# Kernel optimization log

Hardware: AMD Instinct MI355X
Metric: run time of the kernel (lower is better)

## Reference

```python
import jax, jax.numpy as jnp
import numpy as np

D, DK, DV, H, DFF = 1024, 64, 64, 16, 4096
B, LD, LE = 8, 1024, 1024
NEG = -1e9


def _ln(x, g, b, eps=1e-5):
    m = jnp.mean(x, axis=-1, keepdims=True)
    v = jnp.var(x, axis=-1, keepdims=True)
    return (x - m) / jnp.sqrt(v + eps) * g + b


def _mha(q_src, kv_src, wq, bq, wk, bk, wv, bv, mask):
    # wq/wk: [H, D, DK], wv: [H, D, DV]; per-head linear projections (with bias)
    Q = jnp.einsum('bld,hdk->bhlk', q_src, wq) + bq[:, None, :]
    K = jnp.einsum('bld,hdk->bhlk', kv_src, wk) + bk[:, None, :]
    V = jnp.einsum('bld,hdv->bhlv', kv_src, wv) + bv[:, None, :]
    s = jnp.einsum('bhqk,bhmk->bhqm', Q, K) / jnp.sqrt(jnp.asarray(DK, Q.dtype))
    if mask is not None:
        s = s + mask
    a = jax.nn.softmax(s, axis=-1)
    o = jnp.einsum('bhqm,bhmv->bhqv', a, V)  # [B,H,L,DV]
    b_, h_, l_, dv_ = o.shape
    return jnp.transpose(o, (0, 2, 1, 3)).reshape(b_, l_, h_ * dv_)


def setup_inputs() -> dict:
    key = jax.random.key(0)
    ks = jax.random.split(key, 24)
    sc = 0.02
    inp = {
        'decoder_embedding': jax.random.normal(ks[0], (B, LD, D), jnp.float32),
        'encoder_output': jax.random.normal(ks[1], (B, LE, D), jnp.float32),
        # masked (self) attention heads, stacked over H
        'm_wq': jax.random.normal(ks[2], (H, D, DK)) * sc,
        'm_bq': jnp.zeros((H, DK)),
        'm_wk': jax.random.normal(ks[3], (H, D, DK)) * sc,
        'm_bk': jnp.zeros((H, DK)),
        'm_wv': jax.random.normal(ks[4], (H, D, DV)) * sc,
        'm_bv': jnp.zeros((H, DV)),
        # cross attention heads
        'c_wq': jax.random.normal(ks[5], (H, D, DK)) * sc,
        'c_bq': jnp.zeros((H, DK)),
        'c_wk': jax.random.normal(ks[6], (H, D, DK)) * sc,
        'c_bk': jnp.zeros((H, DK)),
        'c_wv': jax.random.normal(ks[7], (H, D, DV)) * sc,
        'c_bv': jnp.zeros((H, DV)),
        # FFN
        'ff_w1': jax.random.normal(ks[8], (D, DFF)) * sc,
        'ff_b1': jnp.zeros((DFF,)),
        'ff_w2': jax.random.normal(ks[9], (DFF, D)) * sc,
        'ff_b2': jnp.zeros((D,)),
        # LayerNorms (ln2 reused for the third norm, as in the source)
        'ln1_g': jnp.ones((D,)), 'ln1_b': jnp.zeros((D,)),
        'ln2_g': jnp.ones((D,)), 'ln2_b': jnp.zeros((D,)),
    }
    return inp


def reference(decoder_embedding, encoder_output,
              m_wq, m_bq, m_wk, m_bk, m_wv, m_bv,
              c_wq, c_bq, c_wk, c_bk, c_wv, c_bv,
              ff_w1, ff_b1, ff_w2, ff_b2,
              ln1_g, ln1_b, ln2_g, ln2_b):
    Ld = decoder_embedding.shape[1]
    causal = jnp.where(jnp.tril(jnp.ones((Ld, Ld), bool)), 0.0, NEG)[None, None]
    # masked self-attention + residual + LN1
    sa = _mha(decoder_embedding, decoder_embedding, m_wq, m_bq, m_wk, m_bk, m_wv, m_bv, causal)
    x = _ln(decoder_embedding + sa, ln1_g, ln1_b)
    # cross-attention (Q from decoder, K/V from encoder) + residual + LN2
    ca = _mha(x, encoder_output, c_wq, c_bq, c_wk, c_bk, c_wv, c_bv, None)
    x = _ln(x + ca, ln2_g, ln2_b)
    # FFN + residual + LN2 again (source reuses layer_norm2)
    ff = jnp.maximum(x @ ff_w1 + ff_b1, 0.0) @ ff_w2 + ff_b2
    return _ln(x + ff, ln2_g, ln2_b)
```

## Files before the change

### kernel.cpp

```cpp
#include <hip/hip_runtime.h>
#include <hip/hip_bf16.h>
#include <cstdint>

typedef __bf16 bf16x8 __attribute__((ext_vector_type(8)));
typedef __bf16 bf16x4 __attribute__((ext_vector_type(4)));
typedef short  short4v __attribute__((ext_vector_type(4)));
typedef _Float16 f16x4 __attribute__((ext_vector_type(4)));
typedef float f32x4 __attribute__((ext_vector_type(4)));

union U128 { uint4 u; __bf16 h[8]; };
union U64  { uint2 u; __bf16 h[4]; };
union PV4  { uint2 u; bf16x4 b; short4v s; f16x4 f; };

#define DMODEL 1024
#define NHEAD  16
#define DHEAD  64

#if __has_builtin(__builtin_amdgcn_mfma_f32_16x16x16_bf16)
#define PV_F16 0
__device__ __forceinline__ f32x4 mfma16(PV4 a, PV4 b, f32x4 c) {
  return __builtin_amdgcn_mfma_f32_16x16x16_bf16(a.b, b.b, c, 0, 0, 0);
}
#elif __has_builtin(__builtin_amdgcn_mfma_f32_16x16x16bf16_1k)
#define PV_F16 0
__device__ __forceinline__ f32x4 mfma16(PV4 a, PV4 b, f32x4 c) {
  return __builtin_amdgcn_mfma_f32_16x16x16bf16_1k(a.s, b.s, c, 0, 0, 0);
}
#else
#define PV_F16 1
__device__ __forceinline__ f32x4 mfma16(PV4 a, PV4 b, f32x4 c) {
  return __builtin_amdgcn_mfma_f32_16x16x16f16(a.f, b.f, c, 0, 0, 0);
}
#endif

__device__ __forceinline__ uint16_t pv_bits(__bf16 v) {
#if PV_F16
  union { _Float16 f; uint16_t u; } x; x.f = (_Float16)(float)v; return x.u;
#else
  union { __bf16 b; uint16_t u; } x; x.b = v; return x.u;
#endif
}

__device__ __forceinline__ PV4 pack4(float a, float b, float c, float d) {
  PV4 r;
#if PV_F16
  r.f = (f16x4){(_Float16)a, (_Float16)b, (_Float16)c, (_Float16)d};
#else
  r.b = (bf16x4){(__bf16)a, (__bf16)b, (__bf16)c, (__bf16)d};
#endif
  return r;
}

__device__ __forceinline__ void async_copy16(const void* g, void* l) {
  __builtin_amdgcn_global_load_lds(
      (const __attribute__((address_space(1))) void*)g,
      (__attribute__((address_space(3))) void*)l, 16, 0, 0);
}

__global__ __launch_bounds__(256) void k_cast(const float* __restrict__ s,
    __bf16* __restrict__ d, int n) {
  int i = (blockIdx.x * 256 + threadIdx.x) * 4;
  if (i < n) {
    float4 v = *(const float4*)(s + i);
    U64 o;
    o.h[0] = (__bf16)v.x; o.h[1] = (__bf16)v.y;
    o.h[2] = (__bf16)v.z; o.h[3] = (__bf16)v.w;
    *(uint2*)(d + i) = o.u;
  }
}

__global__ __launch_bounds__(256) void k_pack(float* __restrict__ dst,
    const float* __restrict__ s0, const float* __restrict__ s1,
    const float* __restrict__ s2, int n) {
  int i = blockIdx.x * 256 + threadIdx.x;
  if (i < n) dst[i] = s0[i];
  else if (i < 2 * n) dst[i] = s1[i - n];
  else if (i < 3 * n) dst[i] = s2[i - 2 * n];
}

__global__ __launch_bounds__(256) void k_transpose(const float* __restrict__ src,
    __bf16* __restrict__ dst, int R, int C) {
  __shared__ __bf16 tile[32][33];
  src += (size_t)blockIdx.z * R * C;
  dst += (size_t)blockIdx.z * R * C;
  int c0 = blockIdx.x * 32, r0 = blockIdx.y * 32;
  int tx = threadIdx.x & 31, ty = threadIdx.x >> 5;
  for (int i = ty; i < 32; i += 8)
    tile[i][tx] = (__bf16)src[(size_t)(r0 + i) * C + (c0 + tx)];
  __syncthreads();
  for (int i = ty; i < 32; i += 8)
    dst[(size_t)(c0 + i) * R + (r0 + tx)] = tile[tx][i];
}

template<bool RELU, typename OutT>
__global__ __launch_bounds__(256, 3) void k_gemm(const __bf16* __restrict__ A,
    const __bf16* __restrict__ Bt, const float* __restrict__ bias,
    OutT* __restrict__ C, int M, int N, int K) {
  __shared__ __bf16 As[128][64];
  __shared__ __bf16 Bs[128][64];
  const int m0 = blockIdx.y * 128, n0 = blockIdx.x * 128;
  const int t = threadIdx.x;
  const int wave = t >> 6, lane = t & 63;
  const int wm = (wave & 1) * 64, wn = (wave >> 1) * 64;
  const int lrow = lane & 15, quad = lane >> 4;
  const int r8 = lane >> 3;
  const int gG = (lane & 7) ^ (r8 & 7);
  const __bf16* Ap[4]; const __bf16* Bp[4];
  __bf16* lA[4]; __bf16* lB[4];
  for (int j = 0; j < 4; j++) {
    int rr = wave * 8 + j * 32 + r8;
    Ap[j] = A  + (size_t)(m0 + rr) * K + gG * 8;
    Bp[j] = Bt + (size_t)(n0 + rr) * K + gG * 8;
    lA[j] = &As[wave * 8 + j * 32][0];
    lB[j] = &Bs[wave * 8 + j * 32][0];
  }
  f32x4 acc[4][4] = {};
  for (int k0 = 0; k0 < K; k0 += 64) {
    __syncthreads();
    for (int j = 0; j < 4; j++) {
      async_copy16(Ap[j] + k0, lA[j]);
      async_copy16(Bp[j] + k0, lB[j]);
    }
    __syncthreads();
    for (int ks = 0; ks < 2; ks++) {
      bf16x8 af[4], bfv[4];
      for (int i = 0; i < 4; i++) {
        int ra = wm + i * 16 + lrow, rb = wn + i * 16 + lrow;
        af[i]  = *(const bf16x8*)&As[ra][(((ks * 4 + quad) ^ (ra & 7))) * 8];
        bfv[i] = *(const bf16x8*)&Bs[rb][(((ks * 4 + quad) ^ (rb & 7))) * 8];
      }
      for (int mi = 0; mi < 4; mi++)
        for (int ni = 0; ni < 4; ni++)
          acc[mi][ni] = __builtin_amdgcn_mfma_f32_16x16x32_bf16(af[mi], bfv[ni], acc[mi][ni], 0, 0, 0);
    }
  }
  for (int ni = 0; ni < 4; ni++) {
    int col = n0 + wn + ni * 16 + lrow;
    float bv = bias[col];
    for (int mi = 0; mi < 4; mi++) {
      int row = m0 + wm + mi * 16 + quad * 4;
      for (int r = 0; r < 4; r++) {
        float v = acc[mi][ni][r] + bv;
        if (RELU) v = fmaxf(v, 0.f);
        C[(size_t)(row + r) * N + col] = (OutT)v;
      }
    }
  }
}

template<bool CAUSAL>
__global__ __launch_bounds__(256, 4) void k_attn(const __bf16* __restrict__ Q,
    const __bf16* __restrict__ Kg, const __bf16* __restrict__ Vg,
    float* __restrict__ O, int Lq, int Lk, int qs, int kvs) {
  __shared__ alignas(16) __bf16   Ks[2][64][72];
  __shared__ alignas(16) uint16_t Vt[2][64][72];
  const int t = threadIdx.x;
  const int wave = t >> 6, lane = t & 63;
  const int lrow = lane & 15, quad = lane >> 4;
  const int wm16 = wave * 16;
  const int qt = CAUSAL ? (gridDim.x - 1 - blockIdx.x) : blockIdx.x;
  const int q0 = qt * 64;
  const int b = blockIdx.y >> 4, h = blockIdx.y & 15;
  const __bf16* Qb = Q  + (size_t)b * Lq * qs  + h * DHEAD;
  const __bf16* Kb = Kg + (size_t)b * Lk * kvs + h * DHEAD;
  const __bf16* Vb = Vg + (size_t)b * Lk * kvs + h * DHEAD;
  bf16x8 qf[2];
  for (int ks = 0; ks < 2; ks++) {
    U128 u;
    u.u = *(const uint4*)(Qb + (size_t)(q0 + wm16 + lrow) * qs + ks * 32 + quad * 8);
    for (int j = 0; j < 8; j++) u.h[j] = (__bf16)((float)u.h[j] * 0.125f);
    qf[ks] = *(const bf16x8*)u.h;
  }
  const int nkt = CAUSAL ? (qt + 1) : (Lk / 64);
  const int krow = t >> 3, kcol = (t & 7) * 8;
  const int vkk = t & 63;
  f32x4 acc_o[4] = {};
  float m_r = -1e30f, l_r = 0.f;
  uint4 ka, ka2, va, va2;
  {
    ka  = *(const uint4*)(Kb + (size_t)krow * kvs + kcol);
    ka2 = *(const uint4*)(Kb + (size_t)(krow + 32) * kvs + kcol);
    va  = *(const uint4*)(Vb + (size_t)vkk * kvs + wave * 8);
    va2 = *(const uint4*)(Vb + (size_t)vkk * kvs + (wave + 4) * 8);
  }
  int c = 0;
  for (int kt = 0; kt < nkt; kt++) {
    const int kn = (kt + 1 < nkt) ? (kt + 1) * 64 : kt * 64;
    uint4 na  = *(const uint4*)(Kb + (size_t)(kn + krow) * kvs + kcol);
    uint4 na2 = *(const uint4*)(Kb + (size_t)(kn + krow + 32) * kvs + kcol);
    uint4 nv  = *(const uint4*)(Vb + (size_t)(kn + vkk) * kvs + wave * 8);
    uint4 nv2 = *(const uint4*)(Vb + (size_t)(kn + vkk) * kvs + (wave + 4) * 8);
    *(uint4*)&Ks[c][krow][kcol]      = ka;
    *(uint4*)&Ks[c][krow + 32][kcol] = ka2;
    { U128 u; u.u = va;  for (int j = 0; j < 8; j++) Vt[c][wave * 8 + j][vkk] = pv_bits(u.h[j]); }
    { U128 u; u.u = va2; for (int j = 0; j < 8; j++) Vt[c][(wave + 4) * 8 + j][vkk] = pv_bits(u.h[j]); }
    __syncthreads();
    f32x4 st[4] = {};
    for (int ks = 0; ks < 2; ks++)
      for (int nb = 0; nb < 4; nb++) {
        bf16x8 kf = *(const bf16x8*)&Ks[c][nb * 16 + lrow][ks * 32 + quad * 8];
        st[nb] = __builtin_amdgcn_mfma_f32_16x16x32_bf16(kf, qf[ks], st[nb], 0, 0, 0);
      }
    float pm = -1e30f;
    for (int nb = 0; nb < 4; nb++)
      for (int r = 0; r < 4; r++) {
        float s = st[nb][r];
        if (CAUSAL && kt == qt)
          if (nb * 16 + quad * 4 + r > wm16 + lrow) s = -1e30f;
        st[nb][r] = s;
        pm = fmaxf(pm, s);
      }
    pm = fmaxf(pm, __shfl_xor(pm, 16));
    pm = fmaxf(pm, __shfl_xor(pm, 32));
    float mn = fmaxf(m_r, pm);
    float alpha = __expf(m_r - mn);
    m_r = mn;
    float rs = 0.f;
    PV4 pf[4];
    for (int nb = 0; nb < 4; nb++) {
      float p0 = __expf(st[nb][0] - mn), p1 = __expf(st[nb][1] - mn);
      float p2 = __expf(st[nb][2] - mn), p3 = __expf(st[nb][3] - mn);
      rs += (p0 + p1) + (p2 + p3);
      pf[nb] = pack4(p0, p1, p2, p3);
    }
    rs += __shfl_xor(rs, 16);
    rs += __shfl_xor(rs, 32);
    l_r = l_r * alpha + rs;
    for (int ni = 0; ni < 4; ni++)
      for (int r = 0; r < 4; r++) acc_o[ni][r] *= alpha;
    for (int nb = 0; nb < 4; nb++)
      for (int ni = 0; ni < 4; ni++) {
        PV4 vf; vf.u = *(const uint2*)&Vt[c][ni * 16 + lrow][nb * 16 + quad * 4];
        acc_o[ni] = mfma16(vf, pf[nb], acc_o[ni]);
      }
    ka = na; ka2 = na2; va = nv; va2 = nv2;
    c ^= 1;
  }
  const float linv = 1.f / fmaxf(l_r, 1e-30f);
  float* orow = O + (size_t)b * Lq * DMODEL + (size_t)(q0 + wm16 + lrow) * DMODEL + h * DHEAD;
  for (int ni = 0; ni < 4; ni++) {
    float4 v = { acc_o[ni][0] * linv, acc_o[ni][1] * linv,
                 acc_o[ni][2] * linv, acc_o[ni][3] * linv };
    *(float4*)(orow + ni * 16 + quad * 4) = v;
  }
}

template<typename ResT, typename OutT>
__global__ __launch_bounds__(256) void k_ln_add(const ResT* __restrict__ a,
    const float* __restrict__ bres, const float* __restrict__ g,
    const float* __restrict__ be, OutT* __restrict__ out) {
  __shared__ float red[2][4];
  const int r = blockIdx.x, t = threadIdx.x;
  const size_t base = (size_t)r * DMODEL + t * 4;
  float x[4];
  for (int i = 0; i < 4; i++) x[i] = (float)a[base + i] + bres[base + i];
  float s  = x[0] + x[1] + x[2] + x[3];
  float s2 = x[0]*x[0] + x[1]*x[1] + x[2]*x[2] + x[3]*x[3];
  for (int off = 32; off > 0; off >>= 1) {
    s  += __shfl_down(s, off);
    s2 += __shfl_down(s2, off);
  }
  if ((t & 63) == 0) { red[0][t >> 6] = s; red[1][t >> 6] = s2; }
  __syncthreads();
  s  = red[0][0] + red[0][1] + red[0][2] + red[0][3];
  s2 = red[1][0] + red[1][1] + red[1][2] + red[1][3];
  const float mean = s * (1.f / DMODEL);
  const float var  = s2 * (1.f / DMODEL) - mean * mean;
  const float rstd = rsqrtf(var + 1e-5f);
  for (int i = 0; i < 4; i++)
    out[base + i] = (OutT)((x[i] - mean) * rstd * g[t * 4 + i] + be[t * 4 + i]);
}

extern "C" void kernel_launch(void* const* d_in, const int* in_sizes, int n_in,
                              void* d_out, int out_size, void* d_ws, size_t ws_size,
                              hipStream_t stream) {
  (void)in_sizes; (void)n_in; (void)out_size; (void)ws_size;
  const float* dec   = (const float*)d_in[0];
  const float* enc   = (const float*)d_in[1];
  const float* m_wq  = (const float*)d_in[2];
  const float* m_bq  = (const float*)d_in[3];
  const float* m_wk  = (const float*)d_in[4];
  const float* m_bk  = (const float*)d_in[5];
  const float* m_wv  = (const float*)d_in[6];
  const float* m_bv  = (const float*)d_in[7];
  const float* c_wq  = (const float*)d_in[8];
  const float* c_bq  = (const float*)d_in[9];
  const float* c_wk  = (const float*)d_in[10];
  const float* c_bk  = (const float*)d_in[11];
  const float* c_wv  = (const float*)d_in[12];
  const float* c_bv  = (const float*)d_in[13];
  const float* ff_w1 = (const float*)d_in[14];
  const float* ff_b1 = (const float*)d_in[15];
  const float* ff_w2 = (const float*)d_in[16];
  const float* ff_b2 = (const float*)d_in[17];
  const float* ln1_g = (const float*)d_in[18];
  const float* ln1_b = (const float*)d_in[19];
  const float* ln2_g = (const float*)d_in[20];
  const float* ln2_b = (const float*)d_in[21];

  char* w = (char*)d_ws;
  __bf16* decB = (__bf16*)(w);
  __bf16* encB = (__bf16*)(w + (16ull << 20));
  __bf16* X1b  = decB;
  __bf16* X2b  = encB;
  __bf16* WB   = (__bf16*)(w + (32ull << 20));
  float*  BP   = (float*) (w + (38ull << 20));
  __bf16* QKV  = (__bf16*)(w + (40ull << 20));
  __bf16* KV   = (__bf16*)(w + (40ull << 20));
  __bf16* Qc   = (__bf16*)(w + (72ull << 20));
  __bf16* FF   = (__bf16*)(w + (40ull << 20));
  float*  AO   = (float*) (w + (104ull << 20));
  float* out = (float*)d_out;

  const int M = 8192, NTOK = M * DMODEL;
  dim3 blk(256);
  dim3 gC(NTOK / 1024);
  dim3 gT6(2, 32, 16);
  dim3 gA(16, 128);
  dim3 gL(M);

  k_cast<<<gC, blk, 0, stream>>>(dec, decB, NTOK);
  k_cast<<<gC, blk, 0, stream>>>(enc, encB, NTOK);

  k_transpose<<<gT6, blk, 0, stream>>>(m_wq, WB, 1024, 64);
  k_transpose<<<gT6, blk, 0, stream>>>(m_wk, WB + (1 << 20), 1024, 64);
  k_transpose<<<gT6, blk, 0, stream>>>(m_wv, WB + (2 << 20), 1024, 64);
  k_pack<<<dim3(12), blk, 0, stream>>>(BP, m_bq, m_bk, m_bv, 1024);
  k_gemm<false, __bf16><<<dim3(24, 64), blk, 0, stream>>>(decB, WB, BP, QKV, M, 3072, 1024);
  k_attn<true><<<gA, blk, 0, stream>>>(QKV, QKV + 1024, QKV + 2048, AO, 1024, 1024, 3072, 3072);
  k_ln_add<float, __bf16><<<gL, blk, 0, stream>>>(dec, AO, ln1_g, ln1_b, X1b);

  k_transpose<<<gT6, blk, 0, stream>>>(c_wk, WB, 1024, 64);
  k_transpose<<<gT6, blk, 0, stream>>>(c_wv, WB + (1 << 20), 1024, 64);
  k_transpose<<<gT6, blk, 0, stream>>>(c_wq, WB + (2 << 20), 1024, 64);
  k_pack<<<dim3(8), blk, 0, stream>>>(BP, c_bk, c_bv, c_bv, 1024);
  k_gemm<false, __bf16><<<dim3(16, 64), blk, 0, stream>>>(encB, WB, BP, KV, M, 2048, 1024);
  k_gemm<false, __bf16><<<dim3(8, 64), blk, 0, stream>>>(X1b, WB + (2 << 20), c_bq, Qc, M, 1024, 1024);
  k_attn<false><<<gA, blk, 0, stream>>>(Qc, KV, KV + 1024, AO, 1024, 1024, 1024, 2048);
  k_ln_add<__bf16, __bf16><<<gL, blk, 0, stream>>>(X1b, AO, ln2_g, ln2_b, X2b);

  k_transpose<<<dim3(128, 32, 1), blk, 0, stream>>>(ff_w1, WB, 1024, 4096);
  k_gemm<true, __bf16><<<dim3(32, 64), blk, 0, stream>>>(X2b, WB, ff_b1, FF, M, 4096, 1024);
  k_transpose<<<dim3(32, 128, 1), blk, 0, stream>>>(ff_w2, WB, 4096, 1024);
  k_gemm<false, float><<<dim3(8, 64), blk, 0, stream>>>(FF, WB, ff_b2, AO, M, 1024, 4096);
  k_ln_add<__bf16, float><<<gL, blk, 0, stream>>>(X2b, AO, ln2_g, ln2_b, out);
}
```

Before: 719.3 us.

## Process two query tiles per attention block and merge cast/transpose launches

The attention kernel now handles two 64-row query tiles per block, so each staged K/V tile feeds both. For the causal case the pair is a short tile and its mirror long tile, which balances work across blocks. Softmax moves to exp2 with log2(e) folded into the Q scale. The two input casts are merged into one launch, and the three per-head weight transposes into one. This halves K/V global loads and LDS staging per query and cuts launch count, but raises register use and halves the attention grid.

Result: faster. 688.3 us (-4.3%).

```diff
diff --git a/kernel.cpp b/kernel.cpp
--- a/kernel.cpp
+++ b/kernel.cpp
@@ -57,16 +57,17 @@
       (__attribute__((address_space(3))) void*)l, 16, 0, 0);
 }
 
-__global__ __launch_bounds__(256) void k_cast(const float* __restrict__ s,
-    __bf16* __restrict__ d, int n) {
+__global__ __launch_bounds__(256) void k_cast2(const float* __restrict__ a,
+    const float* __restrict__ b, __bf16* __restrict__ da,
+    __bf16* __restrict__ db, int n) {
   int i = (blockIdx.x * 256 + threadIdx.x) * 4;
-  if (i < n) {
-    float4 v = *(const float4*)(s + i);
-    U64 o;
-    o.h[0] = (__bf16)v.x; o.h[1] = (__bf16)v.y;
-    o.h[2] = (__bf16)v.z; o.h[3] = (__bf16)v.w;
-    *(uint2*)(d + i) = o.u;
-  }
+  const float* s = a; __bf16* d = da;
+  if (i >= n) { s = b; d = db; i -= n; }
+  float4 v = *(const float4*)(s + i);
+  U64 o;
+  o.h[0] = (__bf16)v.x; o.h[1] = (__bf16)v.y;
+  o.h[2] = (__bf16)v.z; o.h[3] = (__bf16)v.w;
+  *(uint2*)(d + i) = o.u;
 }
 
 __global__ __launch_bounds__(256) void k_pack(float* __restrict__ dst,
@@ -83,6 +84,23 @@
   __shared__ __bf16 tile[32][33];
   src += (size_t)blockIdx.z * R * C;
   dst += (size_t)blockIdx.z * R * C;
+  int c0 = blockIdx.x * 32, r0 = blockIdx.y * 32;
+  int tx = threadIdx.x & 31, ty = threadIdx.x >> 5;
+  for (int i = ty; i < 32; i += 8)
+    tile[i][tx] = (__bf16)src[(size_t)(r0 + i) * C + (c0 + tx)];
+  __syncthreads();
+  for (int i = ty; i < 32; i += 8)
+    dst[(size_t)(c0 + i) * R + (r0 + tx)] = tile[tx][i];
+}
+
+__global__ __launch_bounds__(256) void k_transpose3(const float* __restrict__ s0,
+    const float* __restrict__ s1, const float* __restrict__ s2,
+    __bf16* __restrict__ dst, int R, int C) {
+  __shared__ __bf16 tile[32][33];
+  int z = blockIdx.z;
+  const float* src = (z < 16) ? s0 : (z < 32) ? s1 : s2;
+  src += (size_t)(z & 15) * R * C;
+  dst += (size_t)z * R * C;
   int c0 = blockIdx.x * 32, r0 = blockIdx.y * 32;
   int tx = threadIdx.x & 31, ty = threadIdx.x >> 5;
   for (int i = ty; i < 32; i += 8)
@@ -158,31 +176,32 @@
   const int wave = t >> 6, lane = t & 63;
   const int lrow = lane & 15, quad = lane >> 4;
   const int wm16 = wave * 16;
-  const int qt = CAUSAL ? (gridDim.x - 1 - blockIdx.x) : blockIdx.x;
-  const int q0 = qt * 64;
+  int qt[2];
+  if (CAUSAL) { qt[0] = blockIdx.x; qt[1] = gridDim.x * 2 - 1 - blockIdx.x; }
+  else        { qt[0] = blockIdx.x * 2; qt[1] = qt[0] + 1; }
   const int b = blockIdx.y >> 4, h = blockIdx.y & 15;
   const __bf16* Qb = Q  + (size_t)b * Lq * qs  + h * DHEAD;
   const __bf16* Kb = Kg + (size_t)b * Lk * kvs + h * DHEAD;
   const __bf16* Vb = Vg + (size_t)b * Lk * kvs + h * DHEAD;
-  bf16x8 qf[2];
-  for (int ks = 0; ks < 2; ks++) {
-    U128 u;
-    u.u = *(const uint4*)(Qb + (size_t)(q0 + wm16 + lrow) * qs + ks * 32 + quad * 8);
-    for (int j = 0; j < 8; j++) u.h[j] = (__bf16)((float)u.h[j] * 0.125f);
-    qf[ks] = *(const bf16x8*)u.h;
-  }
-  const int nkt = CAUSAL ? (qt + 1) : (Lk / 64);
+  const float qsc = 0.125f * 1.44269504f;
+  bf16x8 qf[2][2];
+  for (int f = 0; f < 2; f++)
+    for (int ks = 0; ks < 2; ks++) {
+      U128 u;
+      u.u = *(const uint4*)(Qb + (size_t)(qt[f] * 64 + wm16 + lrow) * qs + ks * 32 + quad * 8);
+      for (int j = 0; j < 8; j++) u.h[j] = (__bf16)((float)u.h[j] * qsc);
+      qf[f][ks] = *(const bf16x8*)u.h;
+    }
+  const int nkt = CAUSAL ? (qt[1] + 1) : (Lk / 64);
   const int krow = t >> 3, kcol = (t & 7) * 8;
   const int vkk = t & 63;
-  f32x4 acc_o[4] = {};
-  float m_r = -1e30f, l_r = 0.f;
+  f32x4 acc_o[2][4] = {};
+  float m_r[2] = {-1e30f, -1e30f}, l_r[2] = {0.f, 0.f};
   uint4 ka, ka2, va, va2;
-  {
-    ka  = *(const uint4*)(Kb + (size_t)krow * kvs + kcol);
-    ka2 = *(const uint4*)(Kb + (size_t)(krow + 32) * kvs + kcol);
-    va  = *(const uint4*)(Vb + (size_t)vkk * kvs + wave * 8);
-    va2 = *(const uint4*)(Vb + (size_t)vkk * kvs + (wave + 4) * 8);
-  }
+  ka  = *(const uint4*)(Kb + (size_t)krow * kvs + kcol);
+  ka2 = *(const uint4*)(Kb + (size_t)(krow + 32) * kvs + kcol);
+  va  = *(const uint4*)(Vb + (size_t)vkk * kvs + wave * 8);
+  va2 = *(const uint4*)(Vb + (size_t)vkk * kvs + (wave + 4) * 8);
   int c = 0;
   for (int kt = 0; kt < nkt; kt++) {
     const int kn = (kt + 1 < nkt) ? (kt + 1) * 64 : kt * 64;
@@ -195,53 +214,59 @@
     { U128 u; u.u = va;  for (int j = 0; j < 8; j++) Vt[c][wave * 8 + j][vkk] = pv_bits(u.h[j]); }
     { U128 u; u.u = va2; for (int j = 0; j < 8; j++) Vt[c][(wave + 4) * 8 + j][vkk] = pv_bits(u.h[j]); }
     __syncthreads();
-    f32x4 st[4] = {};
-    for (int ks = 0; ks < 2; ks++)
+    for (int f = 0; f < 2; f++) {
+      if (CAUSAL && kt > qt[f]) continue;
+      f32x4 st[4] = {};
+      for (int ks = 0; ks < 2; ks++)
+        for (int nb = 0; nb < 4; nb++) {
+          bf16x8 kf = *(const bf16x8*)&Ks[c][nb * 16 + lrow][ks * 32 + quad * 8];
+          st[nb] = __builtin_amdgcn_mfma_f32_16x16x32_bf16(kf, qf[f][ks], st[nb], 0, 0, 0);
+        }
+      float pm = -1e30f;
+      for (int nb = 0; nb < 4; nb++)
+        for (int r = 0; r < 4; r++) {
+          float s = st[nb][r];
+          if (CAUSAL && kt == qt[f])
+            if (nb * 16 + quad * 4 + r > wm16 + lrow) s = -1e30f;
+          st[nb][r] = s;
+          pm = fmaxf(pm, s);
+        }
+      pm = fmaxf(pm, __shfl_xor(pm, 16));
+      pm = fmaxf(pm, __shfl_xor(pm, 32));
+      float mn = fmaxf(m_r[f], pm);
+      float alpha = exp2f(m_r[f] - mn);
+      m_r[f] = mn;
+      float rs = 0.f;
+      PV4 pf[4];
       for (int nb = 0; nb < 4; nb++) {
-        bf16x8 kf = *(const bf16x8*)&Ks[c][nb * 16 + lrow][ks * 32 + quad * 8];
-        st[nb] = __builtin_amdgcn_mfma_f32_16x16x32_bf16(kf, qf[ks], st[nb], 0, 0, 0);
+        float p0 = exp2f(st[nb][0] - mn), p1 = exp2f(st[nb][1] - mn);
+        float p2 = exp2f(st[nb][2] - mn), p3 = exp2f(st[nb][3] - mn);
+        rs += (p0 + p1) + (p2 + p3);
+        pf[nb] = pack4(p0, p1, p2, p3);
       }
-    float pm = -1e30f;
-    for (int nb = 0; nb < 4; nb++)
-      for (int r = 0; r < 4; r++) {
-        float s = st[nb][r];
-        if (CAUSAL && kt == qt)
-          if (nb * 16 + quad * 4 + r > wm16 + lrow) s = -1e30f;
-        st[nb][r] = s;
-        pm = fmaxf(pm, s);
-      }
-    pm = fmaxf(pm, __shfl_xor(pm, 16));
-    pm = fmaxf(pm, __shfl_xor(pm, 32));
-    float mn = fmaxf(m_r, pm);
-    float alpha = __expf(m_r - mn);
-    m_r = mn;
-    float rs = 0.f;
-    PV4 pf[4];
-    for (int nb = 0; nb < 4; nb++) {
-      float p0 = __expf(st[nb][0] - mn), p1 = __expf(st[nb][1] - mn);
-      float p2 = __expf(st[nb][2] - mn), p3 = __expf(st[nb][3] - mn);
-      rs += (p0 + p1) + (p2 + p3);
-      pf[nb] = pack4(p0, p1, p2, p3);
-    }
-    rs += __shfl_xor(rs, 16);
-    rs += __shfl_xor(rs, 32);
-    l_r = l_r * alpha + rs;
-    for (int ni = 0; ni < 4; ni++)
-      for (int r = 0; r < 4; r++) acc_o[ni][r] *= alpha;
-    for (int nb = 0; nb < 4; nb++)
-      for (int ni = 0; ni < 4; ni++) {
-        PV4 vf; vf.u = *(const uint2*)&Vt[c][ni * 16 + lrow][nb * 16 + quad * 4];
-        acc_o[ni] = mfma16(vf, pf[nb], acc_o[ni]);
-      }
+      rs += __shfl_xor(rs, 16);
+      rs += __shfl_xor(rs, 32);
+      l_r[f] = l_r[f] * alpha + rs;
+      for (int ni = 0; ni < 4; ni++)
+        for (int r = 0; r < 4; r++) acc_o[f][ni][r] *= alpha;
+      for (int nb = 0; nb < 4; nb++)
+        for (int ni = 0; ni < 4; ni++) {
+          PV4 vf; vf.u = *(const uint2*)&Vt[c][ni * 16 + lrow][nb * 16 + quad * 4];
+          acc_o[f][ni] = mfma16(vf, pf[nb], acc_o[f][ni]);
+        }
+    }
     ka = na; ka2 = na2; va = nv; va2 = nv2;
     c ^= 1;
   }
-  const float linv = 1.f / fmaxf(l_r, 1e-30f);
-  float* orow = O + (size_t)b * Lq * DMODEL + (size_t)(q0 + wm16 + lrow) * DMODEL + h * DHEAD;
-  for (int ni = 0; ni < 4; ni++) {
-    float4 v = { acc_o[ni][0] * linv, acc_o[ni][1] * linv,
-                 acc_o[ni][2] * linv, acc_o[ni][3] * linv };
-    *(float4*)(orow + ni * 16 + quad * 4) = v;
+  for (int f = 0; f < 2; f++) {
+    const float linv = 1.f / fmaxf(l_r[f], 1e-30f);
+    float* orow = O + (size_t)b * Lq * DMODEL
+                + (size_t)(qt[f] * 64 + wm16 + lrow) * DMODEL + h * DHEAD;
+    for (int ni = 0; ni < 4; ni++) {
+      float4 v = { acc_o[f][ni][0] * linv, acc_o[f][ni][1] * linv,
+                   acc_o[f][ni][2] * linv, acc_o[f][ni][3] * linv };
+      *(float4*)(orow + ni * 16 + quad * 4) = v;
+    }
   }
 }
 
@@ -314,25 +339,19 @@
 
   const int M = 8192, NTOK = M * DMODEL;
   dim3 blk(256);
-  dim3 gC(NTOK / 1024);
-  dim3 gT6(2, 32, 16);
-  dim3 gA(16, 128);
+  dim3 gT3(2, 32, 48);
+  dim3 gA(8, 128);
   dim3 gL(M);
 
-  k_cast<<<gC, blk, 0, stream>>>(dec, decB, NTOK);
-  k_cast<<<gC, blk, 0, stream>>>(enc, encB, NTOK);
-
-  k_transpose<<<gT6, blk, 0, stream>>>(m_wq, WB, 1024, 64);
-  k_transpose<<<gT6, blk, 0, stream>>>(m_wk, WB + (1 << 20), 1024, 64);
-  k_transpose<<<gT6, blk, 0, stream>>>(m_wv, WB + (2 << 20), 1024, 64);
+  k_cast2<<<dim3(2 * NTOK / 1024), blk, 0, stream>>>(dec, enc, decB, encB, NTOK);
+
+  k_transpose3<<<gT3, blk, 0, stream>>>(m_wq, m_wk, m_wv, WB, 1024, 64);
   k_pack<<<dim3(12), blk, 0, stream>>>(BP, m_bq, m_bk, m_bv, 1024);
   k_gemm<false, __bf16><<<dim3(24, 64), blk, 0, stream>>>(decB, WB, BP, QKV, M, 3072, 1024);
   k_attn<true><<<gA, blk, 0, stream>>>(QKV, QKV + 1024, QKV + 2048, AO, 1024, 1024, 3072, 3072);
   k_ln_add<float, __bf16><<<gL, blk, 0, stream>>>(dec, AO, ln1_g, ln1_b, X1b);
 
-  k_transpose<<<gT6, blk, 0, stream>>>(c_wk, WB, 1024, 64);
-  k_transpose<<<gT6, blk, 0, stream>>>(c_wv, WB + (1 << 20), 1024, 64);
-  k_transpose<<<gT6, blk, 0, stream>>>(c_wq, WB + (2 << 20), 1024, 64);
+  k_transpose3<<<gT3, blk, 0, stream>>>(c_wk, c_wv, c_wq, WB, 1024, 64);
   k_pack<<<dim3(8), blk, 0, stream>>>(BP, c_bk, c_bv, c_bv, 1024);
   k_gemm<false, __bf16><<<dim3(16, 64), blk, 0, stream>>>(encB, WB, BP, KV, M, 2048, 1024);
   k_gemm<false, __bf16><<<dim3(8, 64), blk, 0, stream>>>(X1b, WB + (2 << 20), c_bq, Qc, M, 1024, 1024);
```
